# Performance work log

Hardware: AMD Instinct MI355X
Metric: run time of the kernel (lower is better)

## Reference

```python
import jax, jax.numpy as jnp
import numpy as np

B, H, S, E = 8, 50, 512, 128
D = 2 * E  # feature dim of inputs


def setup_inputs() -> dict:
    key = jax.random.key(0)
    ks = jax.random.split(key, 10)
    def lin(kw, kb, fan_in, fan_out):
        lim = 1.0 / np.sqrt(fan_in)
        w = jax.random.uniform(kw, (fan_out, fan_in), jnp.float32, -lim, lim)
        b = jax.random.uniform(kb, (fan_out,), jnp.float32, -lim, lim)
        return w, b
    wc_w, wc_b = lin(ks[0], ks[1], D, D)
    wh_w, wh_b = lin(ks[2], ks[3], D, D)
    qt_w, qt_b = lin(ks[4], ks[5], D, 1)
    wf_w, wf_b = lin(ks[6], ks[7], 2 * D, E)
    return {
        "wca_history_embeddings": jax.random.normal(ks[8], (B, H, S, D), jnp.float32),
        "wca_current_embeddings": jax.random.normal(ks[9], (B, S, D), jnp.float32),
        "wc_w": wc_w, "wc_b": wc_b,
        "wh_w": wh_w, "wh_b": wh_b,
        "qt_w": qt_w, "qt_b": qt_b,
        "wf_w": wf_w, "wf_b": wf_b,
    }


def reference(wca_history_embeddings, wca_current_embeddings,
              wc_w, wc_b, wh_w, wh_b, qt_w, qt_b, wf_w, wf_b):
    # history: [B, H, S, D] -> [B, S, H, D]; current: [B, S, D]
    hist = jnp.transpose(wca_history_embeddings, (0, 2, 1, 3))
    wc_out = wca_current_embeddings @ wc_w.T + wc_b          # [B, S, D]
    wh_out = hist @ wh_w.T + wh_b                             # [B, S, H, D]
    combined = jax.nn.sigmoid(wc_out[:, :, None, :] + wh_out) # [B, S, H, D]
    alpha = combined @ qt_w.T + qt_b                          # [B, S, H, 1]
    history_sum = jnp.sum(alpha * hist, axis=2)               # [B, S, D]
    concat = jnp.concatenate([wca_current_embeddings, history_sum], axis=-1)  # [B, S, 2D]
    return concat @ wf_w.T + wf_b                             # [B, S, E]
```

## Files before the change

kernel.cpp:

```cpp
#include <hip/hip_runtime.h>
#include <hip/hip_bf16.h>

#define Hh 50

typedef __attribute__((ext_vector_type(8))) short bf16x8;
typedef __attribute__((ext_vector_type(4))) float f32x4;

static __device__ __forceinline__ short b16(float x) {
    return __builtin_bit_cast(short, __float2bfloat16(x));
}
static __device__ __forceinline__ bf16x8 cvt8(const float* p) {
    f32x4 a = *(const f32x4*)p;
    f32x4 b = *(const f32x4*)(p + 4);
    bf16x8 r;
    r[0] = b16(a[0]); r[1] = b16(a[1]); r[2] = b16(a[2]); r[3] = b16(a[3]);
    r[4] = b16(b[0]); r[5] = b16(b[1]); r[6] = b16(b[2]); r[7] = b16(b[3]);
    return r;
}

__global__ __launch_bounds__(256) void k_prep(const float* __restrict__ w,
                                              short* __restrict__ o) {
    int t = (int)blockIdx.x * 256 + threadIdx.x;
    int p  = t >> 9;
    int ks = (t >> 6) & 7;
    int l  = t & 63;
    int col = p * 16 + (l & 15);
    int k   = ks * 32 + (l >> 4) * 8;
    bf16x8 v = cvt8(w + (size_t)col * 256 + k);
#pragma unroll
    for (int c = 0; c < 8; c++)
        *(bf16x8*)(o + (size_t)c * 65536 + (size_t)t * 8) = v;
}

__global__ __launch_bounds__(64) void k_wc(const float* __restrict__ cur,
                                           const float* __restrict__ wcw,
                                           const float* __restrict__ wcb,
                                           float* __restrict__ out) {
    int l = threadIdx.x;
    int m0 = (int)(blockIdx.x >> 2) * 16;
    int ntb = (int)(blockIdx.x & 3) * 4;
    int lk = (l >> 4) * 8;

    bf16x8 Af[8];
#pragma unroll
    for (int k = 0; k < 8; k++)
        Af[k] = cvt8(cur + (size_t)(m0 + (l & 15)) * 256 + k * 32 + lk);

#pragma unroll
    for (int nt = 0; nt < 4; nt++) {
        int col = (ntb + nt) * 16 + (l & 15);
        f32x4 a = {0.f, 0.f, 0.f, 0.f};
#pragma unroll
        for (int k = 0; k < 8; k++) {
            bf16x8 Bf = cvt8(wcw + (size_t)col * 256 + k * 32 + lk);
            a = __builtin_amdgcn_mfma_f32_16x16x32_bf16(Af[k], Bf, a, 0, 0, 0);
        }
        float bias = wcb[col];
        int row = m0 + (l >> 4) * 4;
#pragma unroll
        for (int r = 0; r < 4; r++)
            out[(size_t)(row + r) * 256 + col] = a[r] + bias;
    }
}

__global__ __launch_bounds__(256, 3)
void k_main(const float* __restrict__ hist,
            const float* __restrict__ wc_ws,
            const short* __restrict__ whpk,
            const float* __restrict__ whb,
            const float* __restrict__ qtw,
            const float* __restrict__ qtb,
            float* __restrict__ hsum_ws) {
    __shared__ __align__(16) char histA[64 * 512];
    __shared__ float wcrow[256];
    __shared__ float qtl[256];
    __shared__ float alphaP[4][64];
    __shared__ float alphaF[64];

    int tid = threadIdx.x;
    int l = tid & 63;
    int w = tid >> 6;
    int b = (int)(blockIdx.x >> 9);
    int s = (int)(blockIdx.x & 511);
    const short* whq = whpk + (size_t)(blockIdx.x & 7) * 65536;

    for (int c = tid; c < 1600; c += 256) {
        int r = c >> 5, g = c & 31;
        bf16x8 v = cvt8(hist + ((size_t)(b * Hh + r) * 512 + s) * 256 + g * 8);
        *(bf16x8*)(&histA[r * 512 + ((g ^ (r & 15)) << 4)]) = v;
    }
    if (tid < 448) {
        int r = 50 + (tid >> 5), g = tid & 31;
        *(f32x4*)(&histA[r * 512 + ((g ^ (r & 15)) << 4)]) = (f32x4){0.f, 0.f, 0.f, 0.f};
    }
    wcrow[tid] = wc_ws[(size_t)(b * 512 + s) * 256 + tid] + whb[tid];
    qtl[tid] = qtw[tid];
    __syncthreads();

    f32x4 acc[4][4];
#pragma unroll
    for (int m = 0; m < 4; m++)
#pragma unroll
        for (int nt = 0; nt < 4; nt++)
            acc[m][nt] = (f32x4){0.f, 0.f, 0.f, 0.f};

#pragma unroll 1
    for (int half = 0; half < 2; half++) {
        bf16x8 Bh[4][4];
#pragma unroll
        for (int nt = 0; nt < 4; nt++)
#pragma unroll
            for (int kk = 0; kk < 4; kk++) {
                int p = w * 4 + nt;
                int ks = half * 4 + kk;
                Bh[nt][kk] = *(const bf16x8*)(whq + ((size_t)((p * 8 + ks) * 64 + l)) * 8);
            }

#pragma unroll
        for (int kk = 0; kk < 4; kk++) {
            int ks = half * 4 + kk;
            bf16x8 Am[4];
#pragma unroll
            for (int m = 0; m < 4; m++) {
                int rA = m * 16 + (l & 15);
                int g = ks * 4 + (l >> 4);
                Am[m] = *(const bf16x8*)(&histA[rA * 512 + ((g ^ (rA & 15)) << 4)]);
            }
#pragma unroll
            for (int m = 0; m < 4; m++)
#pragma unroll
                for (int nt = 0; nt < 4; nt++)
                    acc[m][nt] = __builtin_amdgcn_mfma_f32_16x16x32_bf16(
                        Am[m], Bh[nt][kk], acc[m][nt], 0, 0, 0);
        }
    }

    float pal[4][4];
#pragma unroll
    for (int m = 0; m < 4; m++)
#pragma unroll
        for (int r = 0; r < 4; r++) pal[m][r] = 0.f;

#pragma unroll
    for (int m = 0; m < 4; m++) {
#pragma unroll
        for (int nt = 0; nt < 4; nt++) {
            int col = w * 64 + nt * 16 + (l & 15);
            float qv = qtl[col], wb = wcrow[col];
#pragma unroll
            for (int r = 0; r < 4; r++) {
                float v = acc[m][nt][r] + wb;
                pal[m][r] += qv * __builtin_amdgcn_rcpf(1.0f + __expf(-v));
            }
        }
    }

#pragma unroll
    for (int m = 0; m < 4; m++) {
#pragma unroll
        for (int r = 0; r < 4; r++) {
            float v = pal[m][r];
            v += __shfl_xor(v, 1);
            v += __shfl_xor(v, 2);
            v += __shfl_xor(v, 4);
            v += __shfl_xor(v, 8);
            if ((l & 15) == 0)
                alphaP[w][m * 16 + (l >> 4) * 4 + r] = v;
        }
    }
    __syncthreads();
    if (tid < Hh)
        alphaF[tid] = qtb[0] + alphaP[0][tid] + alphaP[1][tid] + alphaP[2][tid] + alphaP[3][tid];
    __syncthreads();

    {
        int d = tid;
        float a = 0.f;
#pragma unroll 2
        for (int h = 0; h < Hh; h++) {
            int g = (d >> 3) ^ (h & 15);
            unsigned short u = *(const unsigned short*)(&histA[h * 512 + (g << 4) + (d & 7) * 2]);
            unsigned int x = ((unsigned int)u) << 16;
            a += alphaF[h] * __builtin_bit_cast(float, x);
        }
        hsum_ws[(size_t)(b * 512 + s) * 256 + d] = a;
    }
}

__global__ __launch_bounds__(64) void k_wf(const float* __restrict__ cur,
                                           const float* __restrict__ hsum,
                                           const float* __restrict__ wfw,
                                           const float* __restrict__ wfb,
                                           float* __restrict__ out) {
    int l = threadIdx.x;
    int m0 = (int)(blockIdx.x >> 1) * 16;
    int ntb = (int)(blockIdx.x & 1) * 4;
    int lk = (l >> 4) * 8;

    f32x4 acc[4];
#pragma unroll
    for (int nt = 0; nt < 4; nt++) acc[nt] = (f32x4){0.f, 0.f, 0.f, 0.f};

#pragma unroll
    for (int k = 0; k < 16; k++) {
        int row = m0 + (l & 15);
        bf16x8 Af;
        if (k < 8)
            Af = cvt8(cur + (size_t)row * 256 + k * 32 + lk);
        else
            Af = cvt8(hsum + (size_t)row * 256 + (k - 8) * 32 + lk);
#pragma unroll
        for (int nt = 0; nt < 4; nt++) {
            int col = (ntb + nt) * 16 + (l & 15);
            bf16x8 Bf = cvt8(wfw + (size_t)col * 512 + k * 32 + lk);
            acc[nt] = __builtin_amdgcn_mfma_f32_16x16x32_bf16(Af, Bf, acc[nt], 0, 0, 0);
        }
    }
#pragma unroll
    for (int nt = 0; nt < 4; nt++) {
        int col = (ntb + nt) * 16 + (l & 15);
        float bias = wfb[col];
        int row = m0 + (l >> 4) * 4;
#pragma unroll
        for (int r = 0; r < 4; r++)
            out[(size_t)(row + r) * 128 + col] = acc[nt][r] + bias;
    }
}

extern "C" void kernel_launch(void* const* d_in, const int* in_sizes, int n_in,
                              void* d_out, int out_size, void* d_ws, size_t ws_size,
                              hipStream_t stream) {
    const float* hist = (const float*)d_in[0];
    const float* cur  = (const float*)d_in[1];
    const float* wc_w = (const float*)d_in[2];
    const float* wc_b = (const float*)d_in[3];
    const float* wh_w = (const float*)d_in[4];
    const float* wh_b = (const float*)d_in[5];
    const float* qt_w = (const float*)d_in[6];
    const float* qt_b = (const float*)d_in[7];
    const float* wf_w = (const float*)d_in[8];
    const float* wf_b = (const float*)d_in[9];

    float* wc_ws = (float*)d_ws;
    float* hsum  = (float*)((char*)d_ws + ((size_t)4 << 20));
    short* whpk  = (short*)((char*)d_ws + ((size_t)8 << 20));

    k_prep<<<32, 256, 0, stream>>>(wh_w, whpk);
    k_wc<<<1024, 64, 0, stream>>>(cur, wc_w, wc_b, wc_ws);
    k_main<<<4096, 256, 0, stream>>>(hist, wc_ws, whpk, wh_b, qt_w, qt_b, hsum);
    k_wf<<<512, 64, 0, stream>>>(cur, hsum, wf_w, wf_b, (float*)d_out);
}
```

Baseline: 137.9 us.

## Make k_main persistent over batch with 512 threads and register-resident Wh weights

k_main now launches one 512-thread block per sequence position, which loops over all 8 batches. Each of the 8 waves loads its 32-column slice of the packed Wh weights into registers once and reuses it across batches, so weight fragments are no longer reloaded per block. The history reduction is split across two thread halves and combined through shared memory. In exchange, the grid shrinks from 4096 to 512 blocks. There is no overlap between the history load and compute across batch iterations, and the extra syncs may hurt latency hiding.

```diff
diff --git a/kernel.cpp b/kernel.cpp
--- a/kernel.cpp
+++ b/kernel.cpp
@@ -63,7 +63,7 @@
     }
 }
 
-__global__ __launch_bounds__(256, 3)
+__global__ __launch_bounds__(512, 4)
 void k_main(const float* __restrict__ hist,
             const float* __restrict__ wc_ws,
             const short* __restrict__ whpk,
@@ -74,116 +74,119 @@
     __shared__ __align__(16) char histA[64 * 512];
     __shared__ float wcrow[256];
     __shared__ float qtl[256];
-    __shared__ float alphaP[4][64];
+    __shared__ float alphaP[8][64];
     __shared__ float alphaF[64];
+    __shared__ float hp[2][256];
 
     int tid = threadIdx.x;
     int l = tid & 63;
     int w = tid >> 6;
-    int b = (int)(blockIdx.x >> 9);
-    int s = (int)(blockIdx.x & 511);
+    int s = (int)blockIdx.x;
     const short* whq = whpk + (size_t)(blockIdx.x & 7) * 65536;
 
-    for (int c = tid; c < 1600; c += 256) {
-        int r = c >> 5, g = c & 31;
-        bf16x8 v = cvt8(hist + ((size_t)(b * Hh + r) * 512 + s) * 256 + g * 8);
-        *(bf16x8*)(&histA[r * 512 + ((g ^ (r & 15)) << 4)]) = v;
-    }
-    if (tid < 448) {
-        int r = 50 + (tid >> 5), g = tid & 31;
-        *(f32x4*)(&histA[r * 512 + ((g ^ (r & 15)) << 4)]) = (f32x4){0.f, 0.f, 0.f, 0.f};
-    }
-    wcrow[tid] = wc_ws[(size_t)(b * 512 + s) * 256 + tid] + whb[tid];
-    qtl[tid] = qtw[tid];
-    __syncthreads();
-
-    f32x4 acc[4][4];
-#pragma unroll
-    for (int m = 0; m < 4; m++)
-#pragma unroll
-        for (int nt = 0; nt < 4; nt++)
-            acc[m][nt] = (f32x4){0.f, 0.f, 0.f, 0.f};
+    bf16x8 Bp[2][8];
+#pragma unroll
+    for (int nt2 = 0; nt2 < 2; nt2++)
+#pragma unroll
+        for (int ks = 0; ks < 8; ks++) {
+            int p = w * 2 + nt2;
+            Bp[nt2][ks] = *(const bf16x8*)(whq + ((size_t)((p * 8 + ks) * 64 + l)) * 8);
+        }
 
 #pragma unroll 1
-    for (int half = 0; half < 2; half++) {
-        bf16x8 Bh[4][4];
-#pragma unroll
-        for (int nt = 0; nt < 4; nt++)
-#pragma unroll
-            for (int kk = 0; kk < 4; kk++) {
-                int p = w * 4 + nt;
-                int ks = half * 4 + kk;
-                Bh[nt][kk] = *(const bf16x8*)(whq + ((size_t)((p * 8 + ks) * 64 + l)) * 8);
-            }
-
-#pragma unroll
-        for (int kk = 0; kk < 4; kk++) {
-            int ks = half * 4 + kk;
-            bf16x8 Am[4];
+    for (int b = 0; b < 8; b++) {
+        __syncthreads();
+
+        for (int c = tid; c < 1600; c += 512) {
+            int r = c >> 5, g = c & 31;
+            bf16x8 v = cvt8(hist + ((size_t)(b * Hh + r) * 512 + s) * 256 + g * 8);
+            *(bf16x8*)(&histA[r * 512 + ((g ^ (r & 15)) << 4)]) = v;
+        }
+        if (tid < 448) {
+            int r = 50 + (tid >> 5), g = tid & 31;
+            *(f32x4*)(&histA[r * 512 + ((g ^ (r & 15)) << 4)]) = (f32x4){0.f, 0.f, 0.f, 0.f};
+        }
+        if (tid < 256) {
+            wcrow[tid] = wc_ws[(size_t)(b * 512 + s) * 256 + tid] + whb[tid];
+            qtl[tid] = qtw[tid];
+        }
+        __syncthreads();
+
+        f32x4 acc[4][2];
+#pragma unroll
+        for (int m = 0; m < 4; m++)
+#pragma unroll
+            for (int nt2 = 0; nt2 < 2; nt2++)
+                acc[m][nt2] = (f32x4){0.f, 0.f, 0.f, 0.f};
+
+#pragma unroll
+        for (int ks = 0; ks < 8; ks++) {
 #pragma unroll
             for (int m = 0; m < 4; m++) {
                 int rA = m * 16 + (l & 15);
                 int g = ks * 4 + (l >> 4);
-                Am[m] = *(const bf16x8*)(&histA[rA * 512 + ((g ^ (rA & 15)) << 4)]);
-            }
-#pragma unroll
-            for (int m = 0; m < 4; m++)
-#pragma unroll
-                for (int nt = 0; nt < 4; nt++)
-                    acc[m][nt] = __builtin_amdgcn_mfma_f32_16x16x32_bf16(
-                        Am[m], Bh[nt][kk], acc[m][nt], 0, 0, 0);
-        }
-    }
-
-    float pal[4][4];
-#pragma unroll
-    for (int m = 0; m < 4; m++)
-#pragma unroll
-        for (int r = 0; r < 4; r++) pal[m][r] = 0.f;
-
-#pragma unroll
-    for (int m = 0; m < 4; m++) {
-#pragma unroll
-        for (int nt = 0; nt < 4; nt++) {
-            int col = w * 64 + nt * 16 + (l & 15);
-            float qv = qtl[col], wb = wcrow[col];
+                bf16x8 Am = *(const bf16x8*)(&histA[rA * 512 + ((g ^ (rA & 15)) << 4)]);
+#pragma unroll
+                for (int nt2 = 0; nt2 < 2; nt2++)
+                    acc[m][nt2] = __builtin_amdgcn_mfma_f32_16x16x32_bf16(
+                        Am, Bp[nt2][ks], acc[m][nt2], 0, 0, 0);
+            }
+        }
+
+        float pal[4][4];
+#pragma unroll
+        for (int m = 0; m < 4; m++)
+#pragma unroll
+            for (int r = 0; r < 4; r++) pal[m][r] = 0.f;
+
+#pragma unroll
+        for (int m = 0; m < 4; m++)
+#pragma unroll
+            for (int nt2 = 0; nt2 < 2; nt2++) {
+                int col = w * 32 + nt2 * 16 + (l & 15);
+                float qv = qtl[col], wb = wcrow[col];
+#pragma unroll
+                for (int r = 0; r < 4; r++) {
+                    float v = acc[m][nt2][r] + wb;
+                    pal[m][r] += qv * __builtin_amdgcn_rcpf(1.0f + __expf(-v));
+                }
+            }
+
+#pragma unroll
+        for (int m = 0; m < 4; m++)
 #pragma unroll
             for (int r = 0; r < 4; r++) {
-                float v = acc[m][nt][r] + wb;
-                pal[m][r] += qv * __builtin_amdgcn_rcpf(1.0f + __expf(-v));
-            }
-        }
-    }
-
-#pragma unroll
-    for (int m = 0; m < 4; m++) {
-#pragma unroll
-        for (int r = 0; r < 4; r++) {
-            float v = pal[m][r];
-            v += __shfl_xor(v, 1);
-            v += __shfl_xor(v, 2);
-            v += __shfl_xor(v, 4);
-            v += __shfl_xor(v, 8);
-            if ((l & 15) == 0)
-                alphaP[w][m * 16 + (l >> 4) * 4 + r] = v;
-        }
-    }
-    __syncthreads();
-    if (tid < Hh)
-        alphaF[tid] = qtb[0] + alphaP[0][tid] + alphaP[1][tid] + alphaP[2][tid] + alphaP[3][tid];
-    __syncthreads();
-
-    {
-        int d = tid;
-        float a = 0.f;
-#pragma unroll 2
-        for (int h = 0; h < Hh; h++) {
-            int g = (d >> 3) ^ (h & 15);
-            unsigned short u = *(const unsigned short*)(&histA[h * 512 + (g << 4) + (d & 7) * 2]);
-            unsigned int x = ((unsigned int)u) << 16;
-            a += alphaF[h] * __builtin_bit_cast(float, x);
-        }
-        hsum_ws[(size_t)(b * 512 + s) * 256 + d] = a;
+                float v = pal[m][r];
+                v += __shfl_xor(v, 1);
+                v += __shfl_xor(v, 2);
+                v += __shfl_xor(v, 4);
+                v += __shfl_xor(v, 8);
+                if ((l & 15) == 0)
+                    alphaP[w][m * 16 + (l >> 4) * 4 + r] = v;
+            }
+        __syncthreads();
+        if (tid < Hh)
+            alphaF[tid] = qtb[0] + alphaP[0][tid] + alphaP[1][tid] + alphaP[2][tid] + alphaP[3][tid]
+                        + alphaP[4][tid] + alphaP[5][tid] + alphaP[6][tid] + alphaP[7][tid];
+        __syncthreads();
+
+        {
+            int d = tid & 255;
+            int half = tid >> 8;
+            float a = 0.f;
+#pragma unroll
+            for (int hh = 0; hh < 25; hh++) {
+                int h = half * 25 + hh;
+                int g = (d >> 3) ^ (h & 15);
+                unsigned short u = *(const unsigned short*)(&histA[h * 512 + (g << 4) + (d & 7) * 2]);
+                unsigned int x = ((unsigned int)u) << 16;
+                a += alphaF[h] * __builtin_bit_cast(float, x);
+            }
+            hp[half][d] = a;
+        }
+        __syncthreads();
+        if (tid < 256)
+            hsum_ws[(size_t)(b * 512 + s) * 256 + tid] = hp[0][tid] + hp[1][tid];
     }
 }
 
@@ -247,6 +250,6 @@
 
     k_prep<<<32, 256, 0, stream>>>(wh_w, whpk);
     k_wc<<<1024, 64, 0, stream>>>(cur, wc_w, wc_b, wc_ws);
-    k_main<<<4096, 256, 0, stream>>>(hist, wc_ws, whpk, wh_b, qt_w, qt_b, hsum);
+    k_main<<<512, 512, 0, stream>>>(hist, wc_ws, whpk, wh_b, qt_w, qt_b, hsum);
     k_wf<<<512, 64, 0, stream>>>(cur, hsum, wf_w, wf_b, (float*)d_out);
 }
```

After: 206.0 us. 49.3% more time.

## Split main kernel into flat-row alpha GEMM and separate history-sum kernel

Applied to the files above, without the earlier changes.

Replaces the per-(b,s) kernel, which padded 50 history rows to 64, with a GEMM over the flattened (b,h,s) rows of the history tensor. It uses 128-row tiles, splits the output columns across two blocks, and double-buffers K chunks in LDS, with the weight tiles fetched via global_load_lds. The alpha partial sums go to a workspace, and a new streaming kernel re-reads fp32 history to form the weighted sum. The wh bias is folded into the wc GEMM epilogue. This removes wasted MFMA work on padding and improves weight reuse, at the cost of reading the large history tensor two to three times instead of once.

```diff
diff --git a/kernel.cpp b/kernel.cpp
--- a/kernel.cpp
+++ b/kernel.cpp
@@ -16,6 +16,11 @@
     r[0] = b16(a[0]); r[1] = b16(a[1]); r[2] = b16(a[2]); r[3] = b16(a[3]);
     r[4] = b16(b[0]); r[5] = b16(b[1]); r[6] = b16(b[2]); r[7] = b16(b[3]);
     return r;
+}
+static __device__ __forceinline__ void gload_lds16(const void* g, void* l) {
+    __builtin_amdgcn_global_load_lds(
+        (const __attribute__((address_space(1))) unsigned int*)g,
+        (__attribute__((address_space(3))) unsigned int*)l, 16, 0, 0);
 }
 
 __global__ __launch_bounds__(256) void k_prep(const float* __restrict__ w,
@@ -35,6 +40,7 @@
 __global__ __launch_bounds__(64) void k_wc(const float* __restrict__ cur,
                                            const float* __restrict__ wcw,
                                            const float* __restrict__ wcb,
+                                           const float* __restrict__ whb,
                                            float* __restrict__ out) {
     int l = threadIdx.x;
     int m0 = (int)(blockIdx.x >> 2) * 16;
@@ -55,7 +61,7 @@
             bf16x8 Bf = cvt8(wcw + (size_t)col * 256 + k * 32 + lk);
             a = __builtin_amdgcn_mfma_f32_16x16x32_bf16(Af[k], Bf, a, 0, 0, 0);
         }
-        float bias = wcb[col];
+        float bias = wcb[col] + whb[col];
         int row = m0 + (l >> 4) * 4;
 #pragma unroll
         for (int r = 0; r < 4; r++)
@@ -63,128 +69,157 @@
     }
 }
 
-__global__ __launch_bounds__(256, 3)
-void k_main(const float* __restrict__ hist,
-            const float* __restrict__ wc_ws,
-            const short* __restrict__ whpk,
-            const float* __restrict__ whb,
-            const float* __restrict__ qtw,
-            const float* __restrict__ qtb,
-            float* __restrict__ hsum_ws) {
-    __shared__ __align__(16) char histA[64 * 512];
-    __shared__ float wcrow[256];
-    __shared__ float qtl[256];
-    __shared__ float alphaP[4][64];
-    __shared__ float alphaF[64];
+__global__ __launch_bounds__(512, 4)
+void k_alpha(const float* __restrict__ hist,
+             const float* __restrict__ wcplus,
+             const short* __restrict__ whpk,
+             const float* __restrict__ qtw,
+             float* __restrict__ aws) {
+    __shared__ __align__(16) char Ab[2][16384];
+    __shared__ __align__(16) char Bb[2][16384];
+    __shared__ float alphaP[2][128];
 
     int tid = threadIdx.x;
     int l = tid & 63;
     int w = tid >> 6;
-    int b = (int)(blockIdx.x >> 9);
-    int s = (int)(blockIdx.x & 511);
-    const short* whq = whpk + (size_t)(blockIdx.x & 7) * 65536;
-
-    for (int c = tid; c < 1600; c += 256) {
-        int r = c >> 5, g = c & 31;
-        bf16x8 v = cvt8(hist + ((size_t)(b * Hh + r) * 512 + s) * 256 + g * 8);
-        *(bf16x8*)(&histA[r * 512 + ((g ^ (r & 15)) << 4)]) = v;
-    }
-    if (tid < 448) {
-        int r = 50 + (tid >> 5), g = tid & 31;
-        *(f32x4*)(&histA[r * 512 + ((g ^ (r & 15)) << 4)]) = (f32x4){0.f, 0.f, 0.f, 0.f};
-    }
-    wcrow[tid] = wc_ws[(size_t)(b * 512 + s) * 256 + tid] + whb[tid];
-    qtl[tid] = qtw[tid];
+    int mh = w >> 1, nh = w & 1;
+    int rt = (int)(blockIdx.x >> 1);
+    int ch = (int)(blockIdx.x & 1);
+    int R0 = rt * 128;
+    int bh = R0 >> 9;
+    int b  = bh / Hh;
+    int s0 = R0 & 511;
+    const short* whq = whpk + (size_t)(rt & 7) * 65536;
+
+    auto stageA = [&](int buf, int c) {
+#pragma unroll
+        for (int p2 = 0; p2 < 2; p2++) {
+            int i = tid + p2 * 512;
+            int row = i >> 3, g3 = i & 7;
+            bf16x8 v = cvt8(hist + (size_t)(R0 + row) * 256 + c * 64 + g3 * 8);
+            *(bf16x8*)(&Ab[buf][row * 128 + ((g3 ^ (row & 7)) << 4)]) = v;
+        }
+    };
+    auto stageB = [&](int buf, int c) {
+        int p = ch * 8 + w;
+#pragma unroll
+        for (int ksl = 0; ksl < 2; ksl++) {
+            const short* g = whq + ((size_t)((p * 8 + c * 2 + ksl) * 64 + l)) * 8;
+            gload_lds16(g, &Bb[buf][(w * 2 + ksl) * 1024]);
+        }
+    };
+
+    stageB(0, 0);
+    stageA(0, 0);
     __syncthreads();
 
-    f32x4 acc[4][4];
-#pragma unroll
-    for (int m = 0; m < 4; m++)
+    f32x4 acc[2][4];
+#pragma unroll
+    for (int mi = 0; mi < 2; mi++)
 #pragma unroll
         for (int nt = 0; nt < 4; nt++)
-            acc[m][nt] = (f32x4){0.f, 0.f, 0.f, 0.f};
+            acc[mi][nt] = (f32x4){0.f, 0.f, 0.f, 0.f};
 
 #pragma unroll 1
-    for (int half = 0; half < 2; half++) {
-        bf16x8 Bh[4][4];
-#pragma unroll
-        for (int nt = 0; nt < 4; nt++)
-#pragma unroll
-            for (int kk = 0; kk < 4; kk++) {
-                int p = w * 4 + nt;
-                int ks = half * 4 + kk;
-                Bh[nt][kk] = *(const bf16x8*)(whq + ((size_t)((p * 8 + ks) * 64 + l)) * 8);
+    for (int c = 0; c < 4; c++) {
+        int buf = c & 1;
+        if (c < 3) {
+            stageB(buf ^ 1, c + 1);
+            stageA(buf ^ 1, c + 1);
+        }
+#pragma unroll
+        for (int ksl = 0; ksl < 2; ksl++) {
+            bf16x8 Am[2], Bf[4];
+#pragma unroll
+            for (int mi = 0; mi < 2; mi++) {
+                int rA = mh * 32 + mi * 16 + (l & 15);
+                int g3 = ksl * 4 + (l >> 4);
+                Am[mi] = *(const bf16x8*)(&Ab[buf][rA * 128 + ((g3 ^ (rA & 7)) << 4)]);
             }
-
-#pragma unroll
-        for (int kk = 0; kk < 4; kk++) {
-            int ks = half * 4 + kk;
-            bf16x8 Am[4];
-#pragma unroll
-            for (int m = 0; m < 4; m++) {
-                int rA = m * 16 + (l & 15);
-                int g = ks * 4 + (l >> 4);
-                Am[m] = *(const bf16x8*)(&histA[rA * 512 + ((g ^ (rA & 15)) << 4)]);
+#pragma unroll
+            for (int nt = 0; nt < 4; nt++)
+                Bf[nt] = *(const bf16x8*)(&Bb[buf][((nh * 4 + nt) * 2 + ksl) * 1024 + l * 16]);
+#pragma unroll
+            for (int mi = 0; mi < 2; mi++)
+#pragma unroll
+                for (int nt = 0; nt < 4; nt++)
+                    acc[mi][nt] = __builtin_amdgcn_mfma_f32_16x16x32_bf16(
+                        Am[mi], Bf[nt], acc[mi][nt], 0, 0, 0);
+        }
+        __syncthreads();
+    }
+
+    float qv[4];
+#pragma unroll
+    for (int nt = 0; nt < 4; nt++)
+        qv[nt] = qtw[ch * 128 + nh * 64 + nt * 16 + (l & 15)];
+
+    float pal[2][4];
+#pragma unroll
+    for (int mi = 0; mi < 2; mi++)
+#pragma unroll
+        for (int r = 0; r < 4; r++) pal[mi][r] = 0.f;
+
+#pragma unroll
+    for (int mi = 0; mi < 2; mi++)
+#pragma unroll
+        for (int nt = 0; nt < 4; nt++) {
+            int col = ch * 128 + nh * 64 + nt * 16 + (l & 15);
+#pragma unroll
+            for (int r = 0; r < 4; r++) {
+                int rl = mh * 32 + mi * 16 + (l >> 4) * 4 + r;
+                float bias = wcplus[(size_t)(b * 512 + s0 + rl) * 256 + col];
+                float v = acc[mi][nt][r] + bias;
+                pal[mi][r] += qv[nt] * __builtin_amdgcn_rcpf(1.0f + __expf(-v));
             }
-#pragma unroll
-            for (int m = 0; m < 4; m++)
-#pragma unroll
-                for (int nt = 0; nt < 4; nt++)
-                    acc[m][nt] = __builtin_amdgcn_mfma_f32_16x16x32_bf16(
-                        Am[m], Bh[nt][kk], acc[m][nt], 0, 0, 0);
-        }
-    }
-
-    float pal[4][4];
-#pragma unroll
-    for (int m = 0; m < 4; m++)
-#pragma unroll
-        for (int r = 0; r < 4; r++) pal[m][r] = 0.f;
-
-#pragma unroll
-    for (int m = 0; m < 4; m++) {
-#pragma unroll
-        for (int nt = 0; nt < 4; nt++) {
-            int col = w * 64 + nt * 16 + (l & 15);
-            float qv = qtl[col], wb = wcrow[col];
-#pragma unroll
-            for (int r = 0; r < 4; r++) {
-                float v = acc[m][nt][r] + wb;
-                pal[m][r] += qv * __builtin_amdgcn_rcpf(1.0f + __expf(-v));
-            }
-        }
-    }
-
-#pragma unroll
-    for (int m = 0; m < 4; m++) {
+        }
+
+#pragma unroll
+    for (int mi = 0; mi < 2; mi++)
 #pragma unroll
         for (int r = 0; r < 4; r++) {
-            float v = pal[m][r];
+            float v = pal[mi][r];
             v += __shfl_xor(v, 1);
             v += __shfl_xor(v, 2);
             v += __shfl_xor(v, 4);
             v += __shfl_xor(v, 8);
             if ((l & 15) == 0)
-                alphaP[w][m * 16 + (l >> 4) * 4 + r] = v;
-        }
-    }
+                alphaP[nh][mh * 32 + mi * 16 + (l >> 4) * 4 + r] = v;
+        }
     __syncthreads();
-    if (tid < Hh)
-        alphaF[tid] = qtb[0] + alphaP[0][tid] + alphaP[1][tid] + alphaP[2][tid] + alphaP[3][tid];
+    if (tid < 128)
+        aws[(size_t)ch * 204800 + R0 + tid] = alphaP[0][tid] + alphaP[1][tid];
+}
+
+__global__ __launch_bounds__(256, 8)
+void k_hsum(const float* __restrict__ hist,
+            const float* __restrict__ aws,
+            const float* __restrict__ qtb,
+            float* __restrict__ hsum) {
+    __shared__ float al[Hh * 4];
+    int tid = threadIdx.x;
+    int b = (int)(blockIdx.x >> 7);
+    int s0 = (int)(blockIdx.x & 127) * 4;
+
+    if (tid < Hh * 4) {
+        int h = tid >> 2, si = tid & 3;
+        size_t row = (size_t)(b * Hh + h) * 512 + s0 + si;
+        al[tid] = qtb[0] + aws[row] + aws[204800 + row];
+    }
     __syncthreads();
 
-    {
-        int d = tid;
-        float a = 0.f;
+    int sl = tid >> 6;
+    int d4 = (tid & 63) * 4;
+    const float* hp = hist + ((size_t)(b * Hh) * 512 + s0 + sl) * 256 + d4;
+    f32x4 a = {0.f, 0.f, 0.f, 0.f};
 #pragma unroll 2
-        for (int h = 0; h < Hh; h++) {
-            int g = (d >> 3) ^ (h & 15);
-            unsigned short u = *(const unsigned short*)(&histA[h * 512 + (g << 4) + (d & 7) * 2]);
-            unsigned int x = ((unsigned int)u) << 16;
-            a += alphaF[h] * __builtin_bit_cast(float, x);
-        }
-        hsum_ws[(size_t)(b * 512 + s) * 256 + d] = a;
-    }
+    for (int h = 0; h < Hh; h++) {
+        f32x4 v = *(const f32x4*)(hp + (size_t)h * 512 * 256);
+        float av = al[h * 4 + sl];
+        a[0] += av * v[0]; a[1] += av * v[1];
+        a[2] += av * v[2]; a[3] += av * v[3];
+    }
+    *(f32x4*)(hsum + ((size_t)(b * 512) + s0 + sl) * 256 + d4) = a;
 }
 
 __global__ __launch_bounds__(64) void k_wf(const float* __restrict__ cur,
@@ -244,9 +279,11 @@
     float* wc_ws = (float*)d_ws;
     float* hsum  = (float*)((char*)d_ws + ((size_t)4 << 20));
     short* whpk  = (short*)((char*)d_ws + ((size_t)8 << 20));
+    float* aws   = (float*)((char*)d_ws + ((size_t)9 << 20));
 
     k_prep<<<32, 256, 0, stream>>>(wh_w, whpk);
-    k_wc<<<1024, 64, 0, stream>>>(cur, wc_w, wc_b, wc_ws);
-    k_main<<<4096, 256, 0, stream>>>(hist, wc_ws, whpk, wh_b, qt_w, qt_b, hsum);
+    k_wc<<<1024, 64, 0, stream>>>(cur, wc_w, wc_b, wh_b, wc_ws);
+    k_alpha<<<3200, 512, 0, stream>>>(hist, wc_ws, whpk, qt_w, aws);
+    k_hsum<<<1024, 256, 0, stream>>>(hist, aws, qt_b, hsum);
     k_wf<<<512, 64, 0, stream>>>(cur, hsum, wf_w, wf_b, (float*)d_out);
 }
```

New measurement: 152.3 us. +10.4%, slower.
